# Kernel optimization log

Hardware: AMD Instinct MI355X
Metric: run time of the kernel (lower is better)

## Reference

```python
import jax, jax.numpy as jnp
import numpy as np

B, S, I, H, F1, C = 1024, 512, 50, 64, 32, 2


def setup_inputs() -> dict:
    key = jax.random.key(0)
    ks = jax.random.split(key, 9)
    s_ih = 1.0 / np.sqrt(H)
    return {
        "x": jax.random.normal(ks[0], (B, S, I), dtype=jnp.float32),
        # PyTorch LSTM params, gate order (i, f, g, o) stacked along dim 0
        "W_ih": jax.random.uniform(ks[1], (4 * H, I), jnp.float32, -s_ih, s_ih),
        "W_hh": jax.random.uniform(ks[2], (4 * H, H), jnp.float32, -s_ih, s_ih),
        "b_ih": jax.random.uniform(ks[3], (4 * H,), jnp.float32, -s_ih, s_ih),
        "b_hh": jax.random.uniform(ks[4], (4 * H,), jnp.float32, -s_ih, s_ih),
        "W1": jax.random.uniform(ks[5], (F1, H), jnp.float32, -s_ih, s_ih),
        "b1": jax.random.uniform(ks[6], (F1,), jnp.float32, -s_ih, s_ih),
        "W2": jax.random.uniform(ks[7], (C, F1), jnp.float32, -1.0 / np.sqrt(F1), 1.0 / np.sqrt(F1)),
        "b2": jax.random.uniform(ks[8], (C,), jnp.float32, -1.0 / np.sqrt(F1), 1.0 / np.sqrt(F1)),
    }


def _lstm_last(x, W_ih, W_hh, b_ih, b_hh):
    # Precompute input contribution for all timesteps in one big GEMM: [B,S,4H]
    xg = jnp.einsum("bsi,gi->bsg", x, W_ih) + b_ih + b_hh
    Bn = x.shape[0]
    Hn = W_hh.shape[1]
    h0 = jnp.zeros((Bn, Hn), dtype=x.dtype)
    c0 = jnp.zeros((Bn, Hn), dtype=x.dtype)

    def step(carry, xt):
        h, c = carry
        g = xt + h @ W_hh.T  # [B,4H]
        i_g, f_g, g_g, o_g = jnp.split(g, 4, axis=-1)
        i_g = jax.nn.sigmoid(i_g)
        f_g = jax.nn.sigmoid(f_g)
        g_g = jnp.tanh(g_g)
        o_g = jax.nn.sigmoid(o_g)
        c_new = f_g * c + i_g * g_g
        h_new = o_g * jnp.tanh(c_new)
        return (h_new, c_new), None

    (h_last, _), _ = jax.lax.scan(step, (h0, c0), xg.transpose(1, 0, 2))
    return h_last  # == out[:, -1, :]


def reference(x, W_ih, W_hh, b_ih, b_hh, W1, b1, W2, b2):
    last_out = _lstm_last(x, W_ih, W_hh, b_ih, b_hh)
    # Dropout is identity in eval mode (deterministic reference)
    h = jax.nn.relu(last_out @ W1.T + b1)
    return h @ W2.T + b2  # [B, num_classes]
```

## Files before the change

kernel.cpp:

```cpp
#include <hip/hip_runtime.h>
#include <math.h>


#define S_LEN  512
#define I_DIM  50
#define H_DIM  64
#define BB     4
#define TC     16
#define NCH    (S_LEN / TC)
#define KROW   40
#define XROW   72
#define XSHALF (BB * TC * XROW)
#define NXE    (BB * TC * I_DIM)
#define F1_DIM 32
#define C_DIM  2
#define ILO    (1.0f / 2048.0f)

typedef __attribute__((ext_vector_type(8))) _Float16 f16x8;
typedef __attribute__((ext_vector_type(4))) float    f32x4;

__device__ __forceinline__ float fast_rcp(float x) { return __builtin_amdgcn_rcpf(x); }
__device__ __forceinline__ float sigm(float v) { return fast_rcp(1.0f + __expf(-v)); }
__device__ __forceinline__ float tanh_fast(float v) {
    return 1.0f - 2.0f * fast_rcp(__expf(2.0f * v) + 1.0f);
}

__device__ __forceinline__ void load_wfrag(const float* __restrict__ Wih,
                                           const float* __restrict__ Whh,
                                           int ktg, int row, int hk,
                                           f16x8& bh, f16x8& bl) {
    #pragma unroll
    for (int j = 0; j < 8; ++j) {
        const int kk = ktg * 32 + hk * 8 + j;
        float wv;
        if (ktg < 2) wv = (kk < I_DIM) ? Wih[row * I_DIM + kk] : 0.0f;
        else         wv = Whh[row * H_DIM + (kk - 64)];
        const _Float16 h = (_Float16)wv;
        bh[j] = h;
        bl[j] = (_Float16)((wv - (float)h) * 2048.0f);
    }
}

#define MFMA16(A, B, C) __builtin_amdgcn_mfma_f32_16x16x32_f16(A, B, C, 0, 0, 0)

#define BAR() do { asm volatile("s_waitcnt lgkmcnt(0)" ::: "memory"); \
                   __builtin_amdgcn_s_barrier(); } while (0)

__global__ __launch_bounds__(512, 1)
void lstm_mfma(const float* __restrict__ x,
               const float* __restrict__ W_ih, const float* __restrict__ W_hh,
               const float* __restrict__ b_ih, const float* __restrict__ b_hh,
               const float* __restrict__ W1,  const float* __restrict__ b1,
               const float* __restrict__ W2,  const float* __restrict__ b2,
               float* __restrict__ out)
{
    __shared__ __align__(16) _Float16 Hst[2][2][16][KROW];
    __shared__ __align__(16) _Float16 Xs[2][BB * TC][XROW];
    __shared__ __align__(16) float    XGb[2][TC][BB][H_DIM][4];
    __shared__ float f1buf[BB][F1_DIM];

    const int u  = threadIdx.x;
    const int w  = u >> 6;
    const int l  = u & 63;
    const int c  = l & 15;
    const int hk = l >> 4;
    const int b0 = blockIdx.x * BB;
    const bool is_scan = (w < 4);
    const int q  = w & 3;
    const f32x4 Z4 = {0.f, 0.f, 0.f, 0.f};

    f16x8 s00h, s00l, s01h, s01l, s10h, s10l, s11h, s11l,
          s20h, s20l, s21h, s21l, s30h, s30l, s31h, s31l;
    f16x8 g00h, g00l, g01h, g01l, g10h, g10l, g11h, g11l,
          g20h, g20l, g21h, g21l, g30h, g30l, g31h, g31l;
    float bs0 = 0.f, bs1 = 0.f, bs2 = 0.f, bs3 = 0.f;
    float cst = 0.0f;

    const float *xp0=x,*xp1=x,*xp2=x,*xp3=x,*xp4=x,*xp5=x,*xp6=x,
                *xp7=x,*xp8=x,*xp9=x,*xp10=x,*xp11=x,*xp12=x;
    int  ld0=0,ld1=0,ld2=0,ld3=0,ld4=0,ld5=0,ld6=0,ld7=0,ld8=0,ld9=0,ld10=0,ld11=0,ld12=0;
    bool v0=false,v1=false,v2=false,v3=false,v4=false,v5=false,v6=false,
         v7=false,v8=false,v9=false,v10=false,v11=false,v12=false;

    if (is_scan) {
        const int base = 16 * w + c;
        load_wfrag(W_ih, W_hh, 2, 0 * H_DIM + base, hk, s00h, s00l);
        load_wfrag(W_ih, W_hh, 3, 0 * H_DIM + base, hk, s01h, s01l);
        load_wfrag(W_ih, W_hh, 2, 1 * H_DIM + base, hk, s10h, s10l);
        load_wfrag(W_ih, W_hh, 3, 1 * H_DIM + base, hk, s11h, s11l);
        load_wfrag(W_ih, W_hh, 2, 2 * H_DIM + base, hk, s20h, s20l);
        load_wfrag(W_ih, W_hh, 3, 2 * H_DIM + base, hk, s21h, s21l);
        load_wfrag(W_ih, W_hh, 2, 3 * H_DIM + base, hk, s30h, s30l);
        load_wfrag(W_ih, W_hh, 3, 3 * H_DIM + base, hk, s31h, s31l);
    } else {
        const int base = 16 * q + c;
        load_wfrag(W_ih, W_hh, 0, 0 * H_DIM + base, hk, g00h, g00l);
        load_wfrag(W_ih, W_hh, 1, 0 * H_DIM + base, hk, g01h, g01l);
        load_wfrag(W_ih, W_hh, 0, 1 * H_DIM + base, hk, g10h, g10l);
        load_wfrag(W_ih, W_hh, 1, 1 * H_DIM + base, hk, g11h, g11l);
        load_wfrag(W_ih, W_hh, 0, 2 * H_DIM + base, hk, g20h, g20l);
        load_wfrag(W_ih, W_hh, 1, 2 * H_DIM + base, hk, g21h, g21l);
        load_wfrag(W_ih, W_hh, 0, 3 * H_DIM + base, hk, g30h, g30l);
        load_wfrag(W_ih, W_hh, 1, 3 * H_DIM + base, hk, g31h, g31l);
        bs0 = b_ih[0 * H_DIM + base] + b_hh[0 * H_DIM + base];
        bs1 = b_ih[1 * H_DIM + base] + b_hh[1 * H_DIM + base];
        bs2 = b_ih[2 * H_DIM + base] + b_hh[2 * H_DIM + base];
        bs3 = b_ih[3 * H_DIM + base] + b_hh[3 * H_DIM + base];

        const int ug = u - 256;
#define PRE(E) { const int idx = ug + (E) * 256; if (idx < NXE) { \
            const int bb_ = idx / (TC * I_DIM); \
            const int rm_ = idx - bb_ * (TC * I_DIM); \
            const int t_  = rm_ / I_DIM; \
            const int ii_ = rm_ - t_ * I_DIM; \
            xp##E = x + (size_t)(b0 + bb_) * (S_LEN * I_DIM) + t_ * I_DIM + ii_; \
            ld##E = (bb_ * TC + t_) * XROW + ii_; v##E = true; } }
        PRE(0) PRE(1) PRE(2) PRE(3) PRE(4) PRE(5) PRE(6)
        PRE(7) PRE(8) PRE(9) PRE(10) PRE(11) PRE(12)
#undef PRE
    }

    for (int i = u; i < 1280; i += 512) ((unsigned*)Hst)[i] = 0u;
    for (int i = u; i < 4608; i += 512) ((unsigned*)Xs)[i]  = 0u;
    __syncthreads();

    if (!is_scan) {
#define STG(E, CH, BUF) if (v##E) { \
        const float t_ = xp##E[(size_t)(CH) * (TC * I_DIM)]; \
        *((_Float16*)Xs + (BUF) * XSHALF + ld##E) = (_Float16)t_; }
        STG(0,0,0) STG(1,0,0) STG(2,0,0) STG(3,0,0) STG(4,0,0) STG(5,0,0)
        STG(6,0,0) STG(7,0,0) STG(8,0,0) STG(9,0,0) STG(10,0,0) STG(11,0,0) STG(12,0,0)
        STG(0,1,1) STG(1,1,1) STG(2,1,1) STG(3,1,1) STG(4,1,1) STG(5,1,1)
        STG(6,1,1) STG(7,1,1) STG(8,1,1) STG(9,1,1) STG(10,1,1) STG(11,1,1) STG(12,1,1)
#undef STG
    }
    __syncthreads();

#define GPK(DB, MT, I) { f32x4 pk; \
    pk[0] = G0[I] + fmaf(ILO, H0[I], bs0); \
    pk[1] = G1[I] + fmaf(ILO, H1[I], bs1); \
    pk[2] = G2[I] + fmaf(ILO, H2[I], bs2); \
    pk[3] = G3[I] + fmaf(ILO, H3[I], bs3); \
    *(f32x4*)&XGb[DB][4 * hk + (I)][MT][16 * q + c][0] = pk; }

#define GEMM_MT(MT, SB, DB) { \
    const f16x8 a0 = *(const f16x8*)&Xs[SB][(MT) * 16 + c][hk * 8]; \
    const f16x8 a1 = *(const f16x8*)&Xs[SB][(MT) * 16 + c][32 + hk * 8]; \
    f32x4 G0 = MFMA16(a0, g00h, Z4); G0 = MFMA16(a1, g01h, G0); \
    f32x4 H0 = MFMA16(a0, g00l, Z4); H0 = MFMA16(a1, g01l, H0); \
    f32x4 G1 = MFMA16(a0, g10h, Z4); G1 = MFMA16(a1, g11h, G1); \
    f32x4 H1 = MFMA16(a0, g10l, Z4); H1 = MFMA16(a1, g11l, H1); \
    f32x4 G2 = MFMA16(a0, g20h, Z4); G2 = MFMA16(a1, g21h, G2); \
    f32x4 H2 = MFMA16(a0, g20l, Z4); H2 = MFMA16(a1, g21l, H2); \
    f32x4 G3 = MFMA16(a0, g30h, Z4); G3 = MFMA16(a1, g31h, G3); \
    f32x4 H3 = MFMA16(a0, g30l, Z4); H3 = MFMA16(a1, g31l, H3); \
    GPK(DB, MT, 0) GPK(DB, MT, 1) GPK(DB, MT, 2) GPK(DB, MT, 3) }

    if (!is_scan) { GEMM_MT(0, 0, 0) GEMM_MT(1, 0, 0) GEMM_MT(2, 0, 0) GEMM_MT(3, 0, 0) }
    __syncthreads();

#define SCAN_STEP(TT, CUR) { \
    const int p = (TT) & 1; \
    const f32x4 xg4 = *(const f32x4*)&XGb[CUR][TT][hk][16 * w + c][0]; \
    const f16x8 ah0 = *(const f16x8*)&Hst[p][0][c][hk * 8]; \
    const f16x8 ah1 = *(const f16x8*)&Hst[p][1][c][hk * 8]; \
    f32x4 A0 = MFMA16(ah0, s00h, Z4); A0 = MFMA16(ah1, s01h, A0); \
    f32x4 L0 = MFMA16(ah0, s00l, Z4); L0 = MFMA16(ah1, s01l, L0); \
    f32x4 A1 = MFMA16(ah0, s10h, Z4); A1 = MFMA16(ah1, s11h, A1); \
    f32x4 L1 = MFMA16(ah0, s10l, Z4); L1 = MFMA16(ah1, s11l, L1); \
    f32x4 A2 = MFMA16(ah0, s20h, Z4); A2 = MFMA16(ah1, s21h, A2); \
    f32x4 L2 = MFMA16(ah0, s20l, Z4); L2 = MFMA16(ah1, s21l, L2); \
    f32x4 A3 = MFMA16(ah0, s30h, Z4); A3 = MFMA16(ah1, s31h, A3); \
    f32x4 L3 = MFMA16(ah0, s30l, Z4); L3 = MFMA16(ah1, s31l, L3); \
    const float p0 = A0[0] + fmaf(ILO, L0[0], xg4[0]); \
    const float p1 = A1[0] + fmaf(ILO, L1[0], xg4[1]); \
    const float p2 = A2[0] + fmaf(ILO, L2[0], xg4[2]); \
    const float p3 = A3[0] + fmaf(ILO, L3[0], xg4[3]); \
    const float gi = sigm(p0), gf = sigm(p1); \
    const float gg = tanh_fast(p2), go = sigm(p3); \
    cst = fmaf(gf, cst, gi * gg); \
    const float hv = go * tanh_fast(cst); \
    const int uo = 16 * w + c; \
    Hst[p ^ 1][uo >> 5][4 * hk][uo & 31] = (_Float16)hv; }

#define XISS(E, CH2) if (v##E) xr##E = xp##E[(size_t)(CH2) * (TC * I_DIM)];
#define XCMT(E, BUF) if (v##E) *((_Float16*)Xs + (BUF) * XSHALF + ld##E) = (_Float16)xr##E;

    for (int ch = 0; ch < NCH; ++ch) {
        const int cur = ch & 1, nx = cur ^ 1;
        const bool cmp = (ch + 1 < NCH);
        const bool stg = (ch + 2 < NCH);
        float xr0=0,xr1=0,xr2=0,xr3=0,xr4=0,xr5=0,xr6=0,
              xr7=0,xr8=0,xr9=0,xr10=0,xr11=0,xr12=0;

        #pragma unroll
        for (int tt = 0; tt < TC; ++tt) {
            if (is_scan) {
                SCAN_STEP(tt, cur)
            } else {
                if (cmp && tt < 4) { GEMM_MT(tt, nx, nx) }
                if (stg) {
                    if (tt == 0) {
                        XISS(0, ch+2) XISS(1, ch+2) XISS(2, ch+2) XISS(3, ch+2)
                        XISS(4, ch+2) XISS(5, ch+2) XISS(6, ch+2) XISS(7, ch+2)
                        XISS(8, ch+2) XISS(9, ch+2) XISS(10, ch+2) XISS(11, ch+2)
                        XISS(12, ch+2)
                    }
                    if (tt == 6)  { XCMT(0, cur)  XCMT(1, cur) }
                    if (tt == 7)  { XCMT(2, cur)  XCMT(3, cur) }
                    if (tt == 8)  { XCMT(4, cur)  XCMT(5, cur) }
                    if (tt == 9)  { XCMT(6, cur)  XCMT(7, cur) }
                    if (tt == 10) { XCMT(8, cur)  XCMT(9, cur) }
                    if (tt == 11) { XCMT(10, cur) XCMT(11, cur) }
                    if (tt == 12) { XCMT(12, cur) }
                }
            }
            BAR();
        }
    }
#undef SCAN_STEP
#undef GEMM_MT
#undef GPK
#undef XISS
#undef XCMT

    __syncthreads();

    if (u < BB * F1_DIM) {
        const int b = u >> 5, f = u & 31;
        float acc = b1[f];
        #pragma unroll
        for (int j = 0; j < H_DIM; ++j) {
            const float hj = (float)Hst[0][j >> 5][4 * b][j & 31];
            acc = fmaf(hj, W1[f * H_DIM + j], acc);
        }
        f1buf[b][f] = fmaxf(acc, 0.0f);
    }
    __syncthreads();
    if (u < BB * C_DIM) {
        const int b = u >> 1, cl = u & 1;
        float acc = b2[cl];
        #pragma unroll
        for (int f = 0; f < F1_DIM; ++f)
            acc = fmaf(f1buf[b][f], W2[cl * F1_DIM + f], acc);
        out[(size_t)(b0 + b) * C_DIM + cl] = acc;
    }
}

extern "C" void kernel_launch(void* const* d_in, const int* in_sizes, int n_in,
                              void* d_out, int out_size, void* d_ws, size_t ws_size,
                              hipStream_t stream) {
    const float* x   = (const float*)d_in[0];
    const float* Wih = (const float*)d_in[1];
    const float* Whh = (const float*)d_in[2];
    const float* bih = (const float*)d_in[3];
    const float* bhh = (const float*)d_in[4];
    const float* W1  = (const float*)d_in[5];
    const float* b1  = (const float*)d_in[6];
    const float* W2  = (const float*)d_in[7];
    const float* b2  = (const float*)d_in[8];
    float* out = (float*)d_out;

    hipLaunchKernelGGL(lstm_mfma, dim3(256), dim3(512), 0, stream,
                       x, Wih, Whh, bih, bhh, W1, b1, W2, b2, out);
}
```

Before: 213.0 us.

## Spread producer GEMM across all timesteps and prioritize scan MFMAs

The producer waves' per-chunk input-projection GEMM, previously done as four large bursts in the first four timesteps, is split into quarter-sized pieces issued one per timestep across all sixteen steps. The scan waves raise their scheduling priority with s_setprio around the recurrent MFMA block, and the xg load is moved after the h-state loads. The aim is to reduce contention between producer and scan waves on the matrix units, which would otherwise stall the latency-critical recurrence. The cost is that partial GEMM accumulators must stay live in registers across barriers, which raises register pressure.

```diff
diff --git a/kernel.cpp b/kernel.cpp
--- a/kernel.cpp
+++ b/kernel.cpp
@@ -75,6 +75,9 @@
           g20h, g20l, g21h, g21l, g30h, g30l, g31h, g31l;
     float bs0 = 0.f, bs1 = 0.f, bs2 = 0.f, bs3 = 0.f;
     float cst = 0.0f;
+
+    f16x8 ga0, ga1;
+    f32x4 G0, H0, G1, H1, G2, H2, G3, H3;
 
     const float *xp0=x,*xp1=x,*xp2=x,*xp3=x,*xp4=x,*xp5=x,*xp6=x,
                 *xp7=x,*xp8=x,*xp9=x,*xp10=x,*xp11=x,*xp12=x;
@@ -143,27 +146,36 @@
     pk[3] = G3[I] + fmaf(ILO, H3[I], bs3); \
     *(f32x4*)&XGb[DB][4 * hk + (I)][MT][16 * q + c][0] = pk; }
 
-#define GEMM_MT(MT, SB, DB) { \
-    const f16x8 a0 = *(const f16x8*)&Xs[SB][(MT) * 16 + c][hk * 8]; \
-    const f16x8 a1 = *(const f16x8*)&Xs[SB][(MT) * 16 + c][32 + hk * 8]; \
-    f32x4 G0 = MFMA16(a0, g00h, Z4); G0 = MFMA16(a1, g01h, G0); \
-    f32x4 H0 = MFMA16(a0, g00l, Z4); H0 = MFMA16(a1, g01l, H0); \
-    f32x4 G1 = MFMA16(a0, g10h, Z4); G1 = MFMA16(a1, g11h, G1); \
-    f32x4 H1 = MFMA16(a0, g10l, Z4); H1 = MFMA16(a1, g11l, H1); \
-    f32x4 G2 = MFMA16(a0, g20h, Z4); G2 = MFMA16(a1, g21h, G2); \
-    f32x4 H2 = MFMA16(a0, g20l, Z4); H2 = MFMA16(a1, g21l, H2); \
-    f32x4 G3 = MFMA16(a0, g30h, Z4); G3 = MFMA16(a1, g31h, G3); \
-    f32x4 H3 = MFMA16(a0, g30l, Z4); H3 = MFMA16(a1, g31l, H3); \
+#define GQ0(SB, MT) { \
+    ga0 = *(const f16x8*)&Xs[SB][(MT) * 16 + c][hk * 8]; \
+    ga1 = *(const f16x8*)&Xs[SB][(MT) * 16 + c][32 + hk * 8]; \
+    G0 = MFMA16(ga0, g00h, Z4); G0 = MFMA16(ga1, g01h, G0); \
+    H0 = MFMA16(ga0, g00l, Z4); H0 = MFMA16(ga1, g01l, H0); }
+#define GQ1() { \
+    G1 = MFMA16(ga0, g10h, Z4); G1 = MFMA16(ga1, g11h, G1); \
+    H1 = MFMA16(ga0, g10l, Z4); H1 = MFMA16(ga1, g11l, H1); }
+#define GQ2() { \
+    G2 = MFMA16(ga0, g20h, Z4); G2 = MFMA16(ga1, g21h, G2); \
+    H2 = MFMA16(ga0, g20l, Z4); H2 = MFMA16(ga1, g21l, H2); }
+#define GQ3(DB, MT) { \
+    G3 = MFMA16(ga0, g30h, Z4); G3 = MFMA16(ga1, g31h, G3); \
+    H3 = MFMA16(ga0, g30l, Z4); H3 = MFMA16(ga1, g31l, H3); \
     GPK(DB, MT, 0) GPK(DB, MT, 1) GPK(DB, MT, 2) GPK(DB, MT, 3) }
 
-    if (!is_scan) { GEMM_MT(0, 0, 0) GEMM_MT(1, 0, 0) GEMM_MT(2, 0, 0) GEMM_MT(3, 0, 0) }
+    if (!is_scan) {
+        GQ0(0, 0) GQ1() GQ2() GQ3(0, 0)
+        GQ0(0, 1) GQ1() GQ2() GQ3(0, 1)
+        GQ0(0, 2) GQ1() GQ2() GQ3(0, 2)
+        GQ0(0, 3) GQ1() GQ2() GQ3(0, 3)
+    }
     __syncthreads();
 
 #define SCAN_STEP(TT, CUR) { \
     const int p = (TT) & 1; \
-    const f32x4 xg4 = *(const f32x4*)&XGb[CUR][TT][hk][16 * w + c][0]; \
     const f16x8 ah0 = *(const f16x8*)&Hst[p][0][c][hk * 8]; \
     const f16x8 ah1 = *(const f16x8*)&Hst[p][1][c][hk * 8]; \
+    const f32x4 xg4 = *(const f32x4*)&XGb[CUR][TT][hk][16 * w + c][0]; \
+    __builtin_amdgcn_s_setprio(1); \
     f32x4 A0 = MFMA16(ah0, s00h, Z4); A0 = MFMA16(ah1, s01h, A0); \
     f32x4 L0 = MFMA16(ah0, s00l, Z4); L0 = MFMA16(ah1, s01l, L0); \
     f32x4 A1 = MFMA16(ah0, s10h, Z4); A1 = MFMA16(ah1, s11h, A1); \
@@ -172,6 +184,7 @@
     f32x4 L2 = MFMA16(ah0, s20l, Z4); L2 = MFMA16(ah1, s21l, L2); \
     f32x4 A3 = MFMA16(ah0, s30h, Z4); A3 = MFMA16(ah1, s31h, A3); \
     f32x4 L3 = MFMA16(ah0, s30l, Z4); L3 = MFMA16(ah1, s31l, L3); \
+    __builtin_amdgcn_s_setprio(0); \
     const float p0 = A0[0] + fmaf(ILO, L0[0], xg4[0]); \
     const float p1 = A1[0] + fmaf(ILO, L1[0], xg4[1]); \
     const float p2 = A2[0] + fmaf(ILO, L2[0], xg4[2]); \
@@ -198,7 +211,13 @@
             if (is_scan) {
                 SCAN_STEP(tt, cur)
             } else {
-                if (cmp && tt < 4) { GEMM_MT(tt, nx, nx) }
+                if (cmp) {
+                    const int mt = tt >> 2, gq = tt & 3;
+                    if (gq == 0) { GQ0(nx, mt) }
+                    if (gq == 1) { GQ1() }
+                    if (gq == 2) { GQ2() }
+                    if (gq == 3) { GQ3(nx, mt) }
+                }
                 if (stg) {
                     if (tt == 0) {
                         XISS(0, ch+2) XISS(1, ch+2) XISS(2, ch+2) XISS(3, ch+2)
@@ -219,7 +238,10 @@
         }
     }
 #undef SCAN_STEP
-#undef GEMM_MT
+#undef GQ0
+#undef GQ1
+#undef GQ2
+#undef GQ3
 #undef GPK
 #undef XISS
 #undef XCMT
```

After: 204.2 us. -4.1%, faster.
